# Optimization experiments

Measured on AMD Instinct MI355X. Metric: run time of the kernel, lower is better.

The kernel has to match this reference:

```python
import jax, jax.numpy as jnp
import numpy as np

N = 100000
E_RAND = 400000
IN_FEATS = 512
HID = 64
HEADS = 8
NUM_CLASSES = 40
SLOPE = 0.2  # DGL GATConv leaky_relu negative_slope


def setup_inputs() -> dict:
    key = jax.random.key(0)
    ks = jax.random.split(key, 12)
    features = jax.random.normal(ks[0], (N, IN_FEATS), dtype=jnp.float32)
    src_r = jax.random.randint(ks[1], (E_RAND,), 0, N)
    dst_r = jax.random.randint(ks[2], (E_RAND,), 0, N)
    loop = jnp.arange(N)
    src = jnp.concatenate([src_r, loop]).astype(jnp.int64)
    dst = jnp.concatenate([dst_r, loop]).astype(jnp.int64)
    def glorot(k, shape, fan_in):
        return jax.random.normal(k, shape, dtype=jnp.float32) * (1.0 / np.sqrt(fan_in))
    W1 = glorot(ks[3], (IN_FEATS, HEADS * HID), IN_FEATS)
    al1 = glorot(ks[4], (HEADS, HID), HID)
    ar1 = glorot(ks[5], (HEADS, HID), HID)
    b1 = jnp.zeros((HEADS * HID,), dtype=jnp.float32)
    W2 = glorot(ks[6], (HEADS * HID, HEADS * NUM_CLASSES), HEADS * HID)
    al2 = glorot(ks[7], (HEADS, NUM_CLASSES), NUM_CLASSES)
    ar2 = glorot(ks[8], (HEADS, NUM_CLASSES), NUM_CLASSES)
    b2 = jnp.zeros((HEADS * NUM_CLASSES,), dtype=jnp.float32)
    return {"features": features, "W1": W1, "al1": al1, "ar1": ar1, "b1": b1,
            "W2": W2, "al2": al2, "ar2": ar2, "b2": b2, "src": src, "dst": dst}


def gat_conv(x, W, al, ar, b, src, dst, heads, d_out):
    # x: [N, F_in] -> feat: [N, H, D]
    n = x.shape[0]
    feat = (x @ W).reshape(n, heads, d_out)
    el = jnp.sum(feat * al, axis=-1)  # [N, H]
    er = jnp.sum(feat * ar, axis=-1)  # [N, H]
    e = jax.nn.leaky_relu(el[src] + er[dst], SLOPE)  # [E, H]
    # segment softmax over incoming edges of each destination node
    emax = jax.ops.segment_max(e, dst, num_segments=n)
    a = jnp.exp(e - emax[dst])
    asum = jax.ops.segment_sum(a, dst, num_segments=n)
    alpha = a / asum[dst]  # [E, H]
    # weighted scatter-sum of source features
    out = jax.ops.segment_sum(feat[src] * alpha[:, :, None], dst, num_segments=n)
    return out + b.reshape(1, heads, d_out)  # [N, H, D]


def reference(features, W1, al1, ar1, b1, W2, al2, ar2, b2, src, dst):
    h = gat_conv(features, W1, al1, ar1, b1, src, dst, HEADS, HID)
    h = jax.nn.relu(h.reshape(N, HEADS * HID))  # flatten(1) + relu; dropout is eval-mode identity
    out = gat_conv(h, W2, al2, ar2, b2, src, dst, HEADS, NUM_CLASSES)
    return out.mean(axis=1)  # [N, num_classes]
```

## Files before the change

kernel.cpp:

```cpp
#include <hip/hip_runtime.h>
#include <cstdint>
#include <cstddef>

#define SLOPE 0.2f
#define HEADS 8

typedef __bf16 bf16_t;
typedef __bf16 bf16x8 __attribute__((ext_vector_type(8)));
typedef float f32x4 __attribute__((ext_vector_type(4)));

__global__ void cvt_a_bf16(const float* __restrict__ in, bf16_t* __restrict__ out, long n8) {
  long gid = (long)blockIdx.x * blockDim.x + threadIdx.x;
  if (gid >= n8) return;
  const float4* ip = (const float4*)in;
  float4 v0 = ip[gid * 2], v1 = ip[gid * 2 + 1];
  bf16x8 o;
  o[0] = (bf16_t)v0.x; o[1] = (bf16_t)v0.y; o[2] = (bf16_t)v0.z; o[3] = (bf16_t)v0.w;
  o[4] = (bf16_t)v1.x; o[5] = (bf16_t)v1.y; o[6] = (bf16_t)v1.z; o[7] = (bf16_t)v1.w;
  ((bf16x8*)out)[gid] = o;
}

__global__ void cvt_w_t(const float* __restrict__ W, bf16_t* __restrict__ Bt, int K, int N) {
  int gid = blockIdx.x * blockDim.x + threadIdx.x;
  if (gid >= K * N) return;
  int nn = gid / K, kk = gid % K;
  Bt[gid] = (bf16_t)W[(size_t)kk * N + nn];
}

__global__ __launch_bounds__(256) void gemm_bf16(
    const bf16_t* __restrict__ A,
    const bf16_t* __restrict__ Bt,
    bf16_t* __restrict__ Cb,
    int M, int Nc, int K) {
  __shared__ __align__(16) unsigned char lds[32768];
  const int tid = threadIdx.x;
  const int wid = tid >> 6, lane = tid & 63;
  const int wm = wid >> 1, wn = wid & 1;
  const int bm = blockIdx.y * 128, bn = blockIdx.x * 128;
  const int quad = lane >> 4, lrow = lane & 15;

  f32x4 acc[4][4] = {};

  const int st_sub = wid * 8 + (lane >> 3);
  const int st_k = 8 * ((lane & 7) ^ (lane >> 3));
  const bf16_t* aSrc = A + (size_t)(bm + st_sub) * K + st_k;
  const bf16_t* bSrc = Bt + (size_t)(bn + st_sub) * K + st_k;

  const int xorv = (lrow & 7) << 4;
  const int aRdBase = (wm * 64 + lrow) * 128;
  const int bRdBase = (wn * 64 + lrow) * 128 + 16384;

  for (int k0 = 0; k0 < K; k0 += 64) {
    if (k0) __syncthreads();
#pragma unroll
    for (int i = 0; i < 4; ++i) {
      __builtin_amdgcn_global_load_lds(
          (const __attribute__((address_space(1))) void*)(aSrc + (size_t)i * 32 * K + k0),
          (__attribute__((address_space(3))) void*)(lds + (i * 4 + wid) * 1024), 16, 0, 0);
    }
#pragma unroll
    for (int i = 0; i < 4; ++i) {
      __builtin_amdgcn_global_load_lds(
          (const __attribute__((address_space(1))) void*)(bSrc + (size_t)i * 32 * K + k0),
          (__attribute__((address_space(3))) void*)(lds + 16384 + (i * 4 + wid) * 1024), 16, 0, 0);
    }
    __syncthreads();
#pragma unroll
    for (int kk = 0; kk < 2; ++kk) {
      bf16x8 af[4], bfr[4];
      const int kb = (kk * 64 + quad * 16) ^ xorv;
#pragma unroll
      for (int mf = 0; mf < 4; ++mf)
        af[mf] = *(const bf16x8*)(lds + aRdBase + mf * 2048 + kb);
#pragma unroll
      for (int nf = 0; nf < 4; ++nf)
        bfr[nf] = *(const bf16x8*)(lds + bRdBase + nf * 2048 + kb);
#pragma unroll
      for (int mf = 0; mf < 4; ++mf)
#pragma unroll
        for (int nf = 0; nf < 4; ++nf)
          acc[mf][nf] =
              __builtin_amdgcn_mfma_f32_16x16x32_bf16(af[mf], bfr[nf], acc[mf][nf], 0, 0, 0);
    }
  }

  const int crow0 = bm + wm * 64 + quad * 4;
  const int ccol0 = bn + wn * 64 + lrow;
#pragma unroll
  for (int mf = 0; mf < 4; ++mf) {
#pragma unroll
    for (int r = 0; r < 4; ++r) {
      int row = crow0 + mf * 16 + r;
      if (row < M) {
#pragma unroll
        for (int nf = 0; nf < 4; ++nf) {
          int col = ccol0 + nf * 16;
          if (col < Nc) Cb[(size_t)row * Nc + col] = (bf16_t)acc[mf][nf][r];
        }
      }
    }
  }
}

__global__ void el_er_b(const bf16_t* __restrict__ featb, const float* __restrict__ al,
                        const float* __restrict__ ar, float* __restrict__ el,
                        float* __restrict__ er, int n, int D) {
  int gid = blockIdx.x * blockDim.x + threadIdx.x;
  if (gid >= n * HEADS) return;
  int node = gid >> 3, h = gid & 7;
  const bf16_t* f = featb + (size_t)node * HEADS * D + h * D;
  const float* alp = al + h * D;
  const float* arp = ar + h * D;
  float a = 0.f, b = 0.f;
  for (int d = 0; d < D; d += 8) {
    bf16x8 v = *(const bf16x8*)(f + d);
#pragma unroll
    for (int i = 0; i < 8; ++i) {
      float x = (float)v[i];
      a = fmaf(x, alp[d + i], a);
      b = fmaf(x, arp[d + i], b);
    }
  }
  el[gid] = a;
  er[gid] = b;
}

__global__ void count_deg(const int* __restrict__ dst, int* __restrict__ deg, int e) {
  int gid = blockIdx.x * blockDim.x + threadIdx.x;
  if (gid < e) atomicAdd(&deg[dst[gid]], 1);
}

__global__ void scan_block(const int* __restrict__ deg, int* __restrict__ incl,
                           int* __restrict__ bsum, int n) {
  __shared__ int tmp[256];
  int t = threadIdx.x;
  int gid = blockIdx.x * 256 + t;
  int v = (gid < n) ? deg[gid] : 0;
  tmp[t] = v;
  __syncthreads();
  for (int off = 1; off < 256; off <<= 1) {
    int x = (t >= off) ? tmp[t - off] : 0;
    __syncthreads();
    tmp[t] += x;
    __syncthreads();
  }
  if (gid < n) incl[gid] = tmp[t];
  if (t == 255) bsum[blockIdx.x] = tmp[255];
}

__global__ void scan_small(const int* __restrict__ bsum, int* __restrict__ bbase, int nb) {
  __shared__ int tmp[512];
  int t = threadIdx.x;
  int v = (t < nb) ? bsum[t] : 0;
  tmp[t] = v;
  __syncthreads();
  for (int off = 1; off < 512; off <<= 1) {
    int x = (t >= off) ? tmp[t - off] : 0;
    __syncthreads();
    tmp[t] += x;
    __syncthreads();
  }
  if (t < nb) bbase[t] = tmp[t] - v;
}

__global__ void finalize_offsets(const int* __restrict__ incl, const int* __restrict__ deg,
                                 const int* __restrict__ bbase, int* __restrict__ offsets,
                                 int n) {
  int gid = blockIdx.x * blockDim.x + threadIdx.x;
  if (gid >= n) return;
  int base = bbase[gid >> 8];
  offsets[gid] = incl[gid] - deg[gid] + base;
  if (gid == n - 1) offsets[n] = incl[gid] + base;
}

__global__ void scatter_edges(const int* __restrict__ src, const int* __restrict__ dst,
                              const int* __restrict__ offsets, int* __restrict__ cursor,
                              int* __restrict__ ssrc, int e) {
  int gid = blockIdx.x * blockDim.x + threadIdx.x;
  if (gid < e) {
    int d = dst[gid];
    int p = offsets[d] + atomicAdd(&cursor[d], 1);
    ssrc[p] = src[gid];
  }
}

__device__ inline void wave_softmax_stats(const float* __restrict__ el, float er_h, int h,
                                          int strip, const int* __restrict__ ssrc, int s0,
                                          int s1, float& m, float& ss) {
  m = -INFINITY;
  ss = 0.f;
  for (int j = s0 + strip; j < s1; j += 8) {
    int s = ssrc[j];
    float x = el[s * HEADS + h] + er_h;
    x = x > 0.f ? x : SLOPE * x;
    if (x > m) {
      ss = ss * __expf(m - x) + 1.f;
      m = x;
    } else {
      ss += __expf(x - m);
    }
  }
#pragma unroll
  for (int mask = 1; mask < 8; mask <<= 1) {
    float mo = __shfl_xor(m, mask, 64);
    float so = __shfl_xor(ss, mask, 64);
    float mn = fmaxf(m, mo);
    float e1 = (m == -INFINITY) ? 0.f : __expf(m - mn);
    float e2 = (mo == -INFINITY) ? 0.f : __expf(mo - mn);
    ss = ss * e1 + so * e2;
    m = mn;
  }
}

__global__ __launch_bounds__(256) void aggregate1(
    const bf16_t* __restrict__ featb, const float* __restrict__ el,
    const float* __restrict__ er, const int* __restrict__ offsets,
    const int* __restrict__ ssrc, const float* __restrict__ bias,
    bf16_t* __restrict__ outb, int n) {
  int wid = threadIdx.x >> 6, lane = threadIdx.x & 63;
  int node = blockIdx.x * 4 + wid;
  if (node >= n) return;
  int s0 = offsets[node], s1 = offsets[node + 1];
  int h = lane >> 3, strip = lane & 7;
  float er_h = er[node * HEADS + h];
  float m, ss;
  wave_softmax_stats(el, er_h, h, strip, ssrc, s0, s1, m, ss);
  float inv_ss = 1.f / ss;

  float acc[8] = {};
  for (int j = s0; j < s1; ++j) {
    int s = ssrc[j];
    float x = el[s * HEADS + h] + er_h;
    x = x > 0.f ? x : SLOPE * x;
    float alpha = __expf(x - m) * inv_ss;
    bf16x8 fv = *(const bf16x8*)(featb + (size_t)s * 512 + lane * 8);
#pragma unroll
    for (int i = 0; i < 8; ++i) acc[i] += alpha * (float)fv[i];
  }
  bf16x8 o;
#pragma unroll
  for (int i = 0; i < 8; ++i) {
    float v = acc[i] + bias[lane * 8 + i];
    o[i] = (bf16_t)fmaxf(v, 0.f);
  }
  *(bf16x8*)(outb + (size_t)node * 512 + lane * 8) = o;
}

__global__ __launch_bounds__(256) void aggregate2(
    const bf16_t* __restrict__ featb, const float* __restrict__ el,
    const float* __restrict__ er, const int* __restrict__ offsets,
    const int* __restrict__ ssrc, const float* __restrict__ bias,
    float* __restrict__ out, int n) {
  __shared__ float red[4][320];
  int wid = threadIdx.x >> 6, lane = threadIdx.x & 63;
  int node = blockIdx.x * 4 + wid;
  if (node >= n) return;
  int s0 = offsets[node], s1 = offsets[node + 1];
  int h = lane >> 3, strip = lane & 7;
  float er_h = er[node * HEADS + h];
  float m, ss;
  wave_softmax_stats(el, er_h, h, strip, ssrc, s0, s1, m, ss);
  float inv_ss = 1.f / ss;

  int alane0 = ((lane + 0 * 64) / 40) * 8;
  int alane1 = ((lane + 1 * 64) / 40) * 8;
  int alane2 = ((lane + 2 * 64) / 40) * 8;
  int alane3 = ((lane + 3 * 64) / 40) * 8;
  int alane4 = ((lane + 4 * 64) / 40) * 8;

  float acc[5] = {};
  for (int j = s0; j < s1; ++j) {
    int s = ssrc[j];
    float x = el[s * HEADS + h] + er_h;
    x = x > 0.f ? x : SLOPE * x;
    float aown = __expf(x - m) * inv_ss;
    const bf16_t* fp = featb + (size_t)s * 320;
    acc[0] += __shfl(aown, alane0, 64) * (float)fp[lane];
    acc[1] += __shfl(aown, alane1, 64) * (float)fp[lane + 64];
    acc[2] += __shfl(aown, alane2, 64) * (float)fp[lane + 128];
    acc[3] += __shfl(aown, alane3, 64) * (float)fp[lane + 192];
    acc[4] += __shfl(aown, alane4, 64) * (float)fp[lane + 256];
  }
#pragma unroll
  for (int k = 0; k < 5; ++k) {
    int d = lane + k * 64;
    red[wid][d] = acc[k] + bias[d];
  }
  __builtin_amdgcn_wave_barrier();
  asm volatile("s_waitcnt lgkmcnt(0)" ::: "memory");
  __builtin_amdgcn_wave_barrier();
  if (lane < 40) {
    float s = 0.f;
#pragma unroll
    for (int hh = 0; hh < HEADS; ++hh) s += red[wid][hh * 40 + lane];
    out[(size_t)node * 40 + lane] = s * 0.125f;
  }
}

extern "C" void kernel_launch(void* const* d_in, const int* in_sizes, int n_in,
                              void* d_out, int out_size, void* d_ws, size_t ws_size,
                              hipStream_t stream) {
  const float* features = (const float*)d_in[0];
  const float* W1 = (const float*)d_in[1];
  const float* al1 = (const float*)d_in[2];
  const float* ar1 = (const float*)d_in[3];
  const float* b1 = (const float*)d_in[4];
  const float* W2 = (const float*)d_in[5];
  const float* al2 = (const float*)d_in[6];
  const float* ar2 = (const float*)d_in[7];
  const float* b2 = (const float*)d_in[8];
  const int* src = (const int*)d_in[9];
  const int* dst = (const int*)d_in[10];
  float* out = (float*)d_out;

  const int n = in_sizes[0] / 512;
  const int e = in_sizes[9];
  const int Mp = ((n + 127) / 128) * 128;

  char* p = (char*)d_ws;
  auto alloc = [&](size_t bytes) {
    char* r = p;
    p += (bytes + 255) & ~(size_t)255;
    return r;
  };
  bf16_t* feat1b = (bf16_t*)alloc((size_t)n * 512 * 2);
  bf16_t* feat2b = feat1b;
  bf16_t* A1b = (bf16_t*)alloc((size_t)Mp * 512 * 2);
  bf16_t* hb = A1b;
  bf16_t* W1t = (bf16_t*)alloc((size_t)512 * 512 * 2);
  bf16_t* W2t = (bf16_t*)alloc((size_t)384 * 512 * 2);
  float* el1 = (float*)alloc((size_t)n * 8 * 4);
  float* er1 = (float*)alloc((size_t)n * 8 * 4);
  float* el2 = (float*)alloc((size_t)n * 8 * 4);
  float* er2 = (float*)alloc((size_t)n * 8 * 4);
  int* deg = (int*)alloc((size_t)n * 4);
  int* cursor = (int*)alloc((size_t)n * 4);
  int* incl = (int*)alloc((size_t)n * 4);
  int* offsets = (int*)alloc((size_t)(n + 1) * 4);
  int nb = (n + 255) / 256;
  int* bsum = (int*)alloc((size_t)nb * 4);
  int* bbase = (int*)alloc((size_t)nb * 4);
  int* ssrc = (int*)alloc((size_t)e * 4);

  hipMemsetAsync(deg, 0, (size_t)n * 4, stream);
  hipMemsetAsync(cursor, 0, (size_t)n * 4, stream);
  hipMemsetAsync(A1b + (size_t)n * 512, 0, (size_t)(Mp - n) * 512 * 2, stream);
  hipMemsetAsync(W2t + (size_t)320 * 512, 0, (size_t)64 * 512 * 2, stream);

  int eb = (e + 255) / 256;
  count_deg<<<eb, 256, 0, stream>>>(dst, deg, e);
  scan_block<<<nb, 256, 0, stream>>>(deg, incl, bsum, n);
  scan_small<<<1, 512, 0, stream>>>(bsum, bbase, nb);
  finalize_offsets<<<nb, 256, 0, stream>>>(incl, deg, bbase, offsets, n);
  scatter_edges<<<eb, 256, 0, stream>>>(src, dst, offsets, cursor, ssrc, e);

  long n8a = (long)n * 512 / 8;
  cvt_a_bf16<<<(int)((n8a + 255) / 256), 256, 0, stream>>>(features, A1b, n8a);
  cvt_w_t<<<(512 * 512 + 255) / 256, 256, 0, stream>>>(W1, W1t, 512, 512);
  cvt_w_t<<<(512 * 320 + 255) / 256, 256, 0, stream>>>(W2, W2t, 512, 320);

  dim3 g1(512 / 128, Mp / 128);
  gemm_bf16<<<g1, 256, 0, stream>>>(A1b, W1t, feat1b, n, 512, 512);
  el_er_b<<<(n * 8 + 255) / 256, 256, 0, stream>>>(feat1b, al1, ar1, el1, er1, n, 64);
  aggregate1<<<(n + 3) / 4, 256, 0, stream>>>(feat1b, el1, er1, offsets, ssrc, b1, hb, n);

  dim3 g2(384 / 128, Mp / 128);
  gemm_bf16<<<g2, 256, 0, stream>>>(hb, W2t, feat2b, n, 320, 512);
  el_er_b<<<(n * 8 + 255) / 256, 256, 0, stream>>>(feat2b, al2, ar2, el2, er2, n, 40);
  aggregate2<<<(n + 3) / 4, 256, 0, stream>>>(feat2b, el2, er2, offsets, ssrc, b2, out, n);
}
```

Before: 528.8 us.

## Fuse fp32-to-bf16 input conversion into GEMM1 and fold el/er into GEMM2

Drops the separate features-to-bf16 conversion pass. GEMM1 now loads fp32 rows directly, converts them in registers and writes to LDS, which saves a full write and re-read of a bf16 copy of the input. For layer 2, W2·al2 and W2·ar2 are precomputed as 16 extra weight columns placed in the padding already present in W2t, so GEMM2 emits el2/er2 directly and the el_er_b pass is removed. The costs are that GEMM1 A-loads become synchronous register loads instead of async global_load_lds, and el2/er2 are now computed from the bf16-rounded h and W-projected vectors, which changes numerics slightly.

```diff
diff --git a/kernel.cpp b/kernel.cpp
--- a/kernel.cpp
+++ b/kernel.cpp
@@ -1,6 +1,7 @@
 #include <hip/hip_runtime.h>
 #include <cstdint>
 #include <cstddef>
+#include <type_traits>
 
 #define SLOPE 0.2f
 #define HEADS 8
@@ -9,17 +10,6 @@
 typedef __bf16 bf16x8 __attribute__((ext_vector_type(8)));
 typedef float f32x4 __attribute__((ext_vector_type(4)));
 
-__global__ void cvt_a_bf16(const float* __restrict__ in, bf16_t* __restrict__ out, long n8) {
-  long gid = (long)blockIdx.x * blockDim.x + threadIdx.x;
-  if (gid >= n8) return;
-  const float4* ip = (const float4*)in;
-  float4 v0 = ip[gid * 2], v1 = ip[gid * 2 + 1];
-  bf16x8 o;
-  o[0] = (bf16_t)v0.x; o[1] = (bf16_t)v0.y; o[2] = (bf16_t)v0.z; o[3] = (bf16_t)v0.w;
-  o[4] = (bf16_t)v1.x; o[5] = (bf16_t)v1.y; o[6] = (bf16_t)v1.z; o[7] = (bf16_t)v1.w;
-  ((bf16x8*)out)[gid] = o;
-}
-
 __global__ void cvt_w_t(const float* __restrict__ W, bf16_t* __restrict__ Bt, int K, int N) {
   int gid = blockIdx.x * blockDim.x + threadIdx.x;
   if (gid >= K * N) return;
@@ -27,11 +17,28 @@
   Bt[gid] = (bf16_t)W[(size_t)kk * N + nn];
 }
 
+__global__ void cvt_wel2(const float* __restrict__ W2, const float* __restrict__ al2,
+                         const float* __restrict__ ar2, bf16_t* __restrict__ W2t) {
+  int gid = blockIdx.x * blockDim.x + threadIdx.x;
+  if (gid >= 8 * 512) return;
+  int h = gid >> 9, k = gid & 511;
+  float a = 0.f, b = 0.f;
+  for (int d = 0; d < 40; ++d) {
+    float w = W2[(size_t)k * 320 + h * 40 + d];
+    a = fmaf(w, al2[h * 40 + d], a);
+    b = fmaf(w, ar2[h * 40 + d], b);
+  }
+  W2t[(size_t)(320 + h) * 512 + k] = (bf16_t)a;
+  W2t[(size_t)(328 + h) * 512 + k] = (bf16_t)b;
+}
+
+template <typename AT, bool HASEL>
 __global__ __launch_bounds__(256) void gemm_bf16(
-    const bf16_t* __restrict__ A,
+    const AT* __restrict__ A,
     const bf16_t* __restrict__ Bt,
     bf16_t* __restrict__ Cb,
-    int M, int Nc, int K) {
+    float* __restrict__ elp, float* __restrict__ erp,
+    int M, int NcFeat, int K) {
   __shared__ __align__(16) unsigned char lds[32768];
   const int tid = threadIdx.x;
   const int wid = tid >> 6, lane = tid & 63;
@@ -43,7 +50,6 @@
 
   const int st_sub = wid * 8 + (lane >> 3);
   const int st_k = 8 * ((lane & 7) ^ (lane >> 3));
-  const bf16_t* aSrc = A + (size_t)(bm + st_sub) * K + st_k;
   const bf16_t* bSrc = Bt + (size_t)(bn + st_sub) * K + st_k;
 
   const int xorv = (lrow & 7) << 4;
@@ -52,11 +58,29 @@
 
   for (int k0 = 0; k0 < K; k0 += 64) {
     if (k0) __syncthreads();
-#pragma unroll
-    for (int i = 0; i < 4; ++i) {
-      __builtin_amdgcn_global_load_lds(
-          (const __attribute__((address_space(1))) void*)(aSrc + (size_t)i * 32 * K + k0),
-          (__attribute__((address_space(3))) void*)(lds + (i * 4 + wid) * 1024), 16, 0, 0);
+    if constexpr (std::is_same<AT, float>::value) {
+#pragma unroll
+      for (int i = 0; i < 4; ++i) {
+        int row = bm + st_sub + i * 32;
+        float4 v0 = make_float4(0.f, 0.f, 0.f, 0.f), v1 = v0;
+        if (row < M) {
+          const float* ap = A + (size_t)row * K + st_k + k0;
+          v0 = *(const float4*)ap;
+          v1 = *(const float4*)(ap + 4);
+        }
+        bf16x8 o;
+        o[0] = (bf16_t)v0.x; o[1] = (bf16_t)v0.y; o[2] = (bf16_t)v0.z; o[3] = (bf16_t)v0.w;
+        o[4] = (bf16_t)v1.x; o[5] = (bf16_t)v1.y; o[6] = (bf16_t)v1.z; o[7] = (bf16_t)v1.w;
+        *(bf16x8*)(lds + (i * 4 + wid) * 1024 + lane * 16) = o;
+      }
+    } else {
+      const bf16_t* aSrc = A + (size_t)(bm + st_sub) * K + st_k;
+#pragma unroll
+      for (int i = 0; i < 4; ++i) {
+        __builtin_amdgcn_global_load_lds(
+            (const __attribute__((address_space(1))) void*)(aSrc + (size_t)i * 32 * K + k0),
+            (__attribute__((address_space(3))) void*)(lds + (i * 4 + wid) * 1024), 16, 0, 0);
+      }
     }
 #pragma unroll
     for (int i = 0; i < 4; ++i) {
@@ -95,7 +119,13 @@
 #pragma unroll
         for (int nf = 0; nf < 4; ++nf) {
           int col = ccol0 + nf * 16;
-          if (col < Nc) Cb[(size_t)row * Nc + col] = (bf16_t)acc[mf][nf][r];
+          float v = acc[mf][nf][r];
+          if (col < NcFeat) {
+            Cb[(size_t)row * NcFeat + col] = (bf16_t)v;
+          } else if (HASEL) {
+            if (col < NcFeat + 8) elp[(size_t)row * 8 + (col - NcFeat)] = v;
+            else if (col < NcFeat + 16) erp[(size_t)row * 8 + (col - NcFeat - 8)] = v;
+          }
         }
       }
     }
@@ -325,8 +355,7 @@
   };
   bf16_t* feat1b = (bf16_t*)alloc((size_t)n * 512 * 2);
   bf16_t* feat2b = feat1b;
-  bf16_t* A1b = (bf16_t*)alloc((size_t)Mp * 512 * 2);
-  bf16_t* hb = A1b;
+  bf16_t* hb = (bf16_t*)alloc((size_t)Mp * 512 * 2);
   bf16_t* W1t = (bf16_t*)alloc((size_t)512 * 512 * 2);
   bf16_t* W2t = (bf16_t*)alloc((size_t)384 * 512 * 2);
   float* el1 = (float*)alloc((size_t)n * 8 * 4);
@@ -344,8 +373,8 @@
 
   hipMemsetAsync(deg, 0, (size_t)n * 4, stream);
   hipMemsetAsync(cursor, 0, (size_t)n * 4, stream);
-  hipMemsetAsync(A1b + (size_t)n * 512, 0, (size_t)(Mp - n) * 512 * 2, stream);
-  hipMemsetAsync(W2t + (size_t)320 * 512, 0, (size_t)64 * 512 * 2, stream);
+  hipMemsetAsync(hb + (size_t)n * 512, 0, (size_t)(Mp - n) * 512 * 2, stream);
+  hipMemsetAsync(W2t + (size_t)336 * 512, 0, (size_t)48 * 512 * 2, stream);
 
   int eb = (e + 255) / 256;
   count_deg<<<eb, 256, 0, stream>>>(dst, deg, e);
@@ -354,18 +383,17 @@
   finalize_offsets<<<nb, 256, 0, stream>>>(incl, deg, bbase, offsets, n);
   scatter_edges<<<eb, 256, 0, stream>>>(src, dst, offsets, cursor, ssrc, e);
 
-  long n8a = (long)n * 512 / 8;
-  cvt_a_bf16<<<(int)((n8a + 255) / 256), 256, 0, stream>>>(features, A1b, n8a);
   cvt_w_t<<<(512 * 512 + 255) / 256, 256, 0, stream>>>(W1, W1t, 512, 512);
   cvt_w_t<<<(512 * 320 + 255) / 256, 256, 0, stream>>>(W2, W2t, 512, 320);
+  cvt_wel2<<<(8 * 512 + 255) / 256, 256, 0, stream>>>(W2, al2, ar2, W2t);
 
   dim3 g1(512 / 128, Mp / 128);
-  gemm_bf16<<<g1, 256, 0, stream>>>(A1b, W1t, feat1b, n, 512, 512);
+  gemm_bf16<float, false><<<g1, 256, 0, stream>>>(features, W1t, feat1b, nullptr, nullptr,
+                                                  n, 512, 512);
   el_er_b<<<(n * 8 + 255) / 256, 256, 0, stream>>>(feat1b, al1, ar1, el1, er1, n, 64);
   aggregate1<<<(n + 3) / 4, 256, 0, stream>>>(feat1b, el1, er1, offsets, ssrc, b1, hb, n);
 
   dim3 g2(384 / 128, Mp / 128);
-  gemm_bf16<<<g2, 256, 0, stream>>>(hb, W2t, feat2b, n, 320, 512);
-  el_er_b<<<(n * 8 + 255) / 256, 256, 0, stream>>>(feat2b, al2, ar2, el2, er2, n, 40);
+  gemm_bf16<bf16_t, true><<<g2, 256, 0, stream>>>(hb, W2t, feat2b, el2, er2, n, 320, 512);
   aggregate2<<<(n + 3) / 4, 256, 0, stream>>>(feat2b, el2, er2, offsets, ssrc, b2, out, n);
 }
```

After: 575.1 us. 1.09x slower.

## Fold layer-2 attention projections into GEMM columns and swizzle GEMM blocks across XCDs

Applied to the files above, without the earlier changes.

Precomputes W2·al2 and W2·ar2 as 16 extra weight columns placed in the padding of the transposed W2, so the second GEMM also writes el2 and er2 directly and the separate el_er_b pass over feat2 is dropped. The GEMM launch changes to a 1D grid with an XCD-aware block remap, so neighbouring tiles land on the same XCD and share L2. el2 and er2 now come from bf16-rounded folded weights, which changes their rounding slightly.

```diff
diff --git a/kernel.cpp b/kernel.cpp
--- a/kernel.cpp
+++ b/kernel.cpp
@@ -27,16 +27,37 @@
   Bt[gid] = (bf16_t)W[(size_t)kk * N + nn];
 }
 
+__global__ void cvt_wel2(const float* __restrict__ W2, const float* __restrict__ al2,
+                         const float* __restrict__ ar2, bf16_t* __restrict__ W2t) {
+  int gid = blockIdx.x * blockDim.x + threadIdx.x;
+  if (gid >= 8 * 512) return;
+  int h = gid >> 9, k = gid & 511;
+  float a = 0.f, b = 0.f;
+  for (int d = 0; d < 40; ++d) {
+    float w = W2[(size_t)k * 320 + h * 40 + d];
+    a = fmaf(w, al2[h * 40 + d], a);
+    b = fmaf(w, ar2[h * 40 + d], b);
+  }
+  W2t[(size_t)(320 + h) * 512 + k] = (bf16_t)a;
+  W2t[(size_t)(328 + h) * 512 + k] = (bf16_t)b;
+}
+
+template <bool HASEL>
 __global__ __launch_bounds__(256) void gemm_bf16(
     const bf16_t* __restrict__ A,
     const bf16_t* __restrict__ Bt,
     bf16_t* __restrict__ Cb,
-    int M, int Nc, int K) {
+    float* __restrict__ elp, float* __restrict__ erp,
+    int M, int NcFeat, int K, int NXT) {
   __shared__ __align__(16) unsigned char lds[32768];
   const int tid = threadIdx.x;
   const int wid = tid >> 6, lane = tid & 63;
   const int wm = wid >> 1, wn = wid & 1;
-  const int bm = blockIdx.y * 128, bn = blockIdx.x * 128;
+  const int nwg = gridDim.x;
+  const int q = nwg >> 3, r = nwg & 7;
+  const int xcd = blockIdx.x & 7, idx = blockIdx.x >> 3;
+  const int swz = (xcd < r ? xcd * (q + 1) : r * (q + 1) + (xcd - r) * q) + idx;
+  const int bm = (swz / NXT) * 128, bn = (swz % NXT) * 128;
   const int quad = lane >> 4, lrow = lane & 15;
 
   f32x4 acc[4][4] = {};
@@ -89,13 +110,19 @@
 #pragma unroll
   for (int mf = 0; mf < 4; ++mf) {
 #pragma unroll
-    for (int r = 0; r < 4; ++r) {
-      int row = crow0 + mf * 16 + r;
+    for (int r2 = 0; r2 < 4; ++r2) {
+      int row = crow0 + mf * 16 + r2;
       if (row < M) {
 #pragma unroll
         for (int nf = 0; nf < 4; ++nf) {
           int col = ccol0 + nf * 16;
-          if (col < Nc) Cb[(size_t)row * Nc + col] = (bf16_t)acc[mf][nf][r];
+          float v = acc[mf][nf][r2];
+          if (col < NcFeat) {
+            Cb[(size_t)row * NcFeat + col] = (bf16_t)v;
+          } else if (HASEL) {
+            if (col < NcFeat + 8) elp[(size_t)row * 8 + (col - NcFeat)] = v;
+            else if (col < NcFeat + 16) erp[(size_t)row * 8 + (col - NcFeat - 8)] = v;
+          }
         }
       }
     }
@@ -345,7 +372,7 @@
   hipMemsetAsync(deg, 0, (size_t)n * 4, stream);
   hipMemsetAsync(cursor, 0, (size_t)n * 4, stream);
   hipMemsetAsync(A1b + (size_t)n * 512, 0, (size_t)(Mp - n) * 512 * 2, stream);
-  hipMemsetAsync(W2t + (size_t)320 * 512, 0, (size_t)64 * 512 * 2, stream);
+  hipMemsetAsync(W2t + (size_t)336 * 512, 0, (size_t)48 * 512 * 2, stream);
 
   int eb = (e + 255) / 256;
   count_deg<<<eb, 256, 0, stream>>>(dst, deg, e);
@@ -358,14 +385,16 @@
   cvt_a_bf16<<<(int)((n8a + 255) / 256), 256, 0, stream>>>(features, A1b, n8a);
   cvt_w_t<<<(512 * 512 + 255) / 256, 256, 0, stream>>>(W1, W1t, 512, 512);
   cvt_w_t<<<(512 * 320 + 255) / 256, 256, 0, stream>>>(W2, W2t, 512, 320);
-
-  dim3 g1(512 / 128, Mp / 128);
-  gemm_bf16<<<g1, 256, 0, stream>>>(A1b, W1t, feat1b, n, 512, 512);
+  cvt_wel2<<<(8 * 512 + 255) / 256, 256, 0, stream>>>(W2, al2, ar2, W2t);
+
+  int nwg1 = (512 / 128) * (Mp / 128);
+  gemm_bf16<false><<<nwg1, 256, 0, stream>>>(A1b, W1t, feat1b, nullptr, nullptr,
+                                             n, 512, 512, 512 / 128);
   el_er_b<<<(n * 8 + 255) / 256, 256, 0, stream>>>(feat1b, al1, ar1, el1, er1, n, 64);
   aggregate1<<<(n + 3) / 4, 256, 0, stream>>>(feat1b, el1, er1, offsets, ssrc, b1, hb, n);
 
-  dim3 g2(384 / 128, Mp / 128);
-  gemm_bf16<<<g2, 256, 0, stream>>>(hb, W2t, feat2b, n, 320, 512);
-  el_er_b<<<(n * 8 + 255) / 256, 256, 0, stream>>>(feat2b, al2, ar2, el2, er2, n, 40);
+  int nwg2 = (384 / 128) * (Mp / 128);
+  gemm_bf16<true><<<nwg2, 256, 0, stream>>>(hb, W2t, feat2b, el2, er2,
+                                            n, 320, 512, 384 / 128);
   aggregate2<<<(n + 3) / 4, 256, 0, stream>>>(feat2b, el2, er2, offsets, ssrc, b2, out, n);
 }
```

New measurement: 526.8 us. Within noise of the previous version (-0.4%).
